# Performance work log

Measured on AMD Instinct MI355X. Metric: run time of the kernel, lower is better.

Reference implementation:

```python
import jax, jax.numpy as jnp
import numpy as np

B, N, K, CIN, COUT = 8, 65536, 16, 3, 64


def setup_inputs() -> dict:
    key = jax.random.key(0)
    k1, k2, k3 = jax.random.split(key, 3)
    return {
        "x": jax.random.normal(k1, (B, N, CIN), dtype=jnp.float32),
        "kernel_points": jax.random.normal(k2, (K, 3), dtype=jnp.float32),
        "weights": jax.random.normal(k3, (K, CIN, COUT), dtype=jnp.float32),
        "sigma": jnp.float32(1.0),
    }


def reference(x, kernel_points, weights, sigma):
    # squared distance from each point to each kernel point: [B, N, K]
    diff = x[:, :, None, :] - kernel_points[None, None, :, :]  # [B, N, K, 3]
    d2 = jnp.sum(diff * diff, axis=-1)
    g = jnp.exp(-0.5 * d2 / (sigma * sigma))  # gaussian correlation [B, N, K]
    # out[b,n,o] = sum_k g[b,n,k] * sum_i x[b,n,i] * W[k,i,o]
    return jnp.einsum("bnk,bni,kio->bno", g, x, weights)
```

## Files before the change

kernel.cpp:

```cpp
#include <hip/hip_runtime.h>


typedef __bf16  bf16x8 __attribute__((ext_vector_type(8)));
typedef float   f32x4  __attribute__((ext_vector_type(4)));

union OctU { unsigned short s[8]; bf16x8 v; };

#define STG_STRIDE 68

__global__ __launch_bounds__(256) void kpconv_mfma(
    const float* __restrict__ x,
    const float* __restrict__ kp,
    const float* __restrict__ w,
    const float* __restrict__ sigma,
    float* __restrict__ out)
{
    __shared__ float stg[4 * 16 * STG_STRIDE];

    const int tid  = threadIdx.x;
    const int lane = tid & 63;
    const int wv   = tid >> 6;
    const int q    = lane >> 4;
    const int n16  = lane & 15;
    const long long base = (long long)blockIdx.x * 256;

    float* const swv = &stg[wv * 16 * STG_STRIDE];

    float kpt[4][3];
#pragma unroll
    for (int e = 0; e < 4; ++e) {
        const int kpi = (e >> 1) * 8 + 2 * q + (e & 1);
#pragma unroll
        for (int d = 0; d < 3; ++d) kpt[e][d] = kp[kpi * 3 + d];
    }

    bf16x8 bfrag[2][4];
#pragma unroll
    for (int h = 0; h < 2; ++h) {
#pragma unroll
        for (int ot = 0; ot < 4; ++ot) {
            OctU o;
#pragma unroll
            for (int j = 0; j < 8; ++j) {
                float v = 0.0f;
                if (j < 6) {
                    const int kpi = h * 8 + 2 * q + (j >= 3);
                    const int i   = (j >= 3) ? (j - 3) : j;
                    v = w[(kpi * 3 + i) * 64 + ot * 16 + n16];
                }
                o.v[j] = (__bf16)v;
            }
            bfrag[h][ot] = o.v;
        }
    }

    const float sg = sigma[0];
    const float scale = -0.72134752f / (sg * sg);

    float xv[4][3];
#pragma unroll
    for (int t4 = 0; t4 < 4; ++t4) {
        const long long p = base + wv * 64 + t4 * 16 + n16;
#pragma unroll
        for (int d = 0; d < 3; ++d) xv[t4][d] = x[p * 3 + d];
    }

#pragma unroll
    for (int t4 = 0; t4 < 4; ++t4) {
        float g[4];
#pragma unroll
        for (int e = 0; e < 4; ++e) {
            const float dx = xv[t4][0] - kpt[e][0];
            const float dy = xv[t4][1] - kpt[e][1];
            const float dz = xv[t4][2] - kpt[e][2];
            g[e] = exp2f((dx * dx + dy * dy + dz * dz) * scale);
        }
        OctU a0, a1;
#pragma unroll
        for (int j = 0; j < 3; ++j) {
            a0.v[j]     = (__bf16)(g[0] * xv[t4][j]);
            a0.v[j + 3] = (__bf16)(g[1] * xv[t4][j]);
            a1.v[j]     = (__bf16)(g[2] * xv[t4][j]);
            a1.v[j + 3] = (__bf16)(g[3] * xv[t4][j]);
        }
        a0.v[6] = a0.v[7] = (__bf16)0.0f;
        a1.v[6] = a1.v[7] = (__bf16)0.0f;

        f32x4 acc[4];
#pragma unroll
        for (int ot = 0; ot < 4; ++ot) {
            acc[ot] = (f32x4){0.f, 0.f, 0.f, 0.f};
            acc[ot] = __builtin_amdgcn_mfma_f32_16x16x32_bf16(a0.v, bfrag[0][ot], acc[ot], 0, 0, 0);
            acc[ot] = __builtin_amdgcn_mfma_f32_16x16x32_bf16(a1.v, bfrag[1][ot], acc[ot], 0, 0, 0);
        }

#pragma unroll
        for (int ot = 0; ot < 4; ++ot) {
#pragma unroll
            for (int r = 0; r < 4; ++r) {
                swv[(q * 4 + r) * STG_STRIDE + ot * 16 + n16] = acc[ot][r];
            }
        }

        const long long trow = base + wv * 64 + t4 * 16;
#pragma unroll
        for (int s = 0; s < 4; ++s) {
            const float* sp = &swv[(s * 4 + q) * STG_STRIDE + n16 * 4];
            f32x4 vv = *reinterpret_cast<const f32x4*>(
                __builtin_assume_aligned(sp, 16));
            float* dp = out + (trow + s * 4 + q) * 64 + n16 * 4;
            *reinterpret_cast<f32x4*>(__builtin_assume_aligned(dp, 16)) = vv;
        }
    }
}

extern "C" void kernel_launch(void* const* d_in, const int* in_sizes, int n_in,
                              void* d_out, int out_size, void* d_ws, size_t ws_size,
                              hipStream_t stream) {
    const float* x     = (const float*)d_in[0];
    const float* kp    = (const float*)d_in[1];
    const float* w     = (const float*)d_in[2];
    const float* sigma = (const float*)d_in[3];
    float* out = (float*)d_out;

    const int npoints = in_sizes[0] / 3;
    const int blocks  = npoints / 256;
    kpconv_mfma<<<blocks, 256, 0, stream>>>(x, kp, w, sigma, out);
}
```

Baseline: 147.9 us.

## Process four point chunks per block with register double-buffered x prefetch

Each block now handles four 256-point chunks instead of one, so the kernel-point and weight fragment setup is amortised over more work. While one chunk is computed, the x values for the next chunk are prefetched into a second register buffer to hide load latency. This cuts the grid size to a quarter (512 blocks for 524288 points), which may reduce occupancy and the amount of parallelism available to hide the output write bandwidth. The output is write-bound at about 134 MB, so any gain depends on better overlap.

```diff
diff --git a/kernel.cpp b/kernel.cpp
--- a/kernel.cpp
+++ b/kernel.cpp
@@ -7,6 +7,7 @@
 union OctU { unsigned short s[8]; bf16x8 v; };
 
 #define STG_STRIDE 68
+#define CHUNKS 4
 
 __global__ __launch_bounds__(256) void kpconv_mfma(
     const float* __restrict__ x,
@@ -22,7 +23,7 @@
     const int wv   = tid >> 6;
     const int q    = lane >> 4;
     const int n16  = lane & 15;
-    const long long base = (long long)blockIdx.x * 256;
+    const long long bbase = (long long)blockIdx.x * (256 * CHUNKS);
 
     float* const swv = &stg[wv * 16 * STG_STRIDE];
 
@@ -57,59 +58,73 @@
     const float sg = sigma[0];
     const float scale = -0.72134752f / (sg * sg);
 
-    float xv[4][3];
+    float xv[2][4][3];
 #pragma unroll
     for (int t4 = 0; t4 < 4; ++t4) {
-        const long long p = base + wv * 64 + t4 * 16 + n16;
+        const long long p = bbase + wv * 64 + t4 * 16 + n16;
 #pragma unroll
-        for (int d = 0; d < 3; ++d) xv[t4][d] = x[p * 3 + d];
+        for (int d = 0; d < 3; ++d) xv[0][t4][d] = x[p * 3 + d];
     }
 
 #pragma unroll
-    for (int t4 = 0; t4 < 4; ++t4) {
-        float g[4];
+    for (int c = 0; c < CHUNKS; ++c) {
+        const int cur = c & 1;
+        const int nxt = cur ^ 1;
+        if (c + 1 < CHUNKS) {
 #pragma unroll
-        for (int e = 0; e < 4; ++e) {
-            const float dx = xv[t4][0] - kpt[e][0];
-            const float dy = xv[t4][1] - kpt[e][1];
-            const float dz = xv[t4][2] - kpt[e][2];
-            g[e] = exp2f((dx * dx + dy * dy + dz * dz) * scale);
+            for (int t4 = 0; t4 < 4; ++t4) {
+                const long long p = bbase + (long long)(c + 1) * 256 + wv * 64 + t4 * 16 + n16;
+#pragma unroll
+                for (int d = 0; d < 3; ++d) xv[nxt][t4][d] = x[p * 3 + d];
+            }
         }
-        OctU a0, a1;
-#pragma unroll
-        for (int j = 0; j < 3; ++j) {
-            a0.v[j]     = (__bf16)(g[0] * xv[t4][j]);
-            a0.v[j + 3] = (__bf16)(g[1] * xv[t4][j]);
-            a1.v[j]     = (__bf16)(g[2] * xv[t4][j]);
-            a1.v[j + 3] = (__bf16)(g[3] * xv[t4][j]);
-        }
-        a0.v[6] = a0.v[7] = (__bf16)0.0f;
-        a1.v[6] = a1.v[7] = (__bf16)0.0f;
-
-        f32x4 acc[4];
-#pragma unroll
-        for (int ot = 0; ot < 4; ++ot) {
-            acc[ot] = (f32x4){0.f, 0.f, 0.f, 0.f};
-            acc[ot] = __builtin_amdgcn_mfma_f32_16x16x32_bf16(a0.v, bfrag[0][ot], acc[ot], 0, 0, 0);
-            acc[ot] = __builtin_amdgcn_mfma_f32_16x16x32_bf16(a1.v, bfrag[1][ot], acc[ot], 0, 0, 0);
-        }
+        const long long cbase = bbase + (long long)c * 256;
 
 #pragma unroll
-        for (int ot = 0; ot < 4; ++ot) {
+        for (int t4 = 0; t4 < 4; ++t4) {
+            float g[4];
 #pragma unroll
-            for (int r = 0; r < 4; ++r) {
-                swv[(q * 4 + r) * STG_STRIDE + ot * 16 + n16] = acc[ot][r];
+            for (int e = 0; e < 4; ++e) {
+                const float dx = xv[cur][t4][0] - kpt[e][0];
+                const float dy = xv[cur][t4][1] - kpt[e][1];
+                const float dz = xv[cur][t4][2] - kpt[e][2];
+                g[e] = exp2f((dx * dx + dy * dy + dz * dz) * scale);
             }
-        }
+            OctU a0, a1;
+#pragma unroll
+            for (int j = 0; j < 3; ++j) {
+                a0.v[j]     = (__bf16)(g[0] * xv[cur][t4][j]);
+                a0.v[j + 3] = (__bf16)(g[1] * xv[cur][t4][j]);
+                a1.v[j]     = (__bf16)(g[2] * xv[cur][t4][j]);
+                a1.v[j + 3] = (__bf16)(g[3] * xv[cur][t4][j]);
+            }
+            a0.v[6] = a0.v[7] = (__bf16)0.0f;
+            a1.v[6] = a1.v[7] = (__bf16)0.0f;
 
-        const long long trow = base + wv * 64 + t4 * 16;
+            f32x4 acc[4];
 #pragma unroll
-        for (int s = 0; s < 4; ++s) {
-            const float* sp = &swv[(s * 4 + q) * STG_STRIDE + n16 * 4];
-            f32x4 vv = *reinterpret_cast<const f32x4*>(
-                __builtin_assume_aligned(sp, 16));
-            float* dp = out + (trow + s * 4 + q) * 64 + n16 * 4;
-            *reinterpret_cast<f32x4*>(__builtin_assume_aligned(dp, 16)) = vv;
+            for (int ot = 0; ot < 4; ++ot) {
+                acc[ot] = (f32x4){0.f, 0.f, 0.f, 0.f};
+                acc[ot] = __builtin_amdgcn_mfma_f32_16x16x32_bf16(a0.v, bfrag[0][ot], acc[ot], 0, 0, 0);
+                acc[ot] = __builtin_amdgcn_mfma_f32_16x16x32_bf16(a1.v, bfrag[1][ot], acc[ot], 0, 0, 0);
+            }
+
+#pragma unroll
+            for (int ot = 0; ot < 4; ++ot) {
+#pragma unroll
+                for (int r = 0; r < 4; ++r) {
+                    swv[(q * 4 + r) * STG_STRIDE + ot * 16 + n16] = acc[ot][r];
+                }
+            }
+            const long long trow = cbase + wv * 64 + t4 * 16;
+#pragma unroll
+            for (int s = 0; s < 4; ++s) {
+                const float* sp = &swv[(s * 4 + q) * STG_STRIDE + n16 * 4];
+                f32x4 vv = *reinterpret_cast<const f32x4*>(
+                    __builtin_assume_aligned(sp, 16));
+                float* dp = out + (trow + s * 4 + q) * 64 + n16 * 4;
+                *reinterpret_cast<f32x4*>(__builtin_assume_aligned(dp, 16)) = vv;
+            }
         }
     }
 }
@@ -124,6 +139,6 @@
     float* out = (float*)d_out;
 
     const int npoints = in_sizes[0] / 3;
-    const int blocks  = npoints / 256;
+    const int blocks  = npoints / (256 * CHUNKS);
     kpconv_mfma<<<blocks, 256, 0, stream>>>(x, kp, w, sigma, out);
 }
```

Measured after the change: 144.5 us. 2.3% less time.
